# Optimization experiments

Hardware: AMD Instinct MI355X
Metric: run time of the kernel (lower is better)

The kernel has to match this reference:

```python
import jax, jax.numpy as jnp
import numpy as np

K = 24            # neighbors
RBF_KERNELS = 16
RBF_GAMMA = 10.0
CUTOFF = 5.0
BN_EPS = 1e-5


def setup_inputs() -> dict:
    key = jax.random.key(0)
    ks = jax.random.split(key, 6)
    B, C, N = 16, 32, 2048
    x = jax.random.normal(ks[0], (B, C, N), dtype=jnp.float32)
    idx_base = (jnp.arange(B, dtype=jnp.int64) * N).reshape(B, 1, 1)
    att_w1 = jax.random.normal(ks[1], (64, 2 * C + RBF_KERNELS), dtype=jnp.float32) * 0.1
    att_w2 = jax.random.normal(ks[2], (1, 64), dtype=jnp.float32) * 0.1
    upd_w = jax.random.normal(ks[3], (64, C), dtype=jnp.float32) * 0.1
    bn_gamma = jnp.ones((64,), dtype=jnp.float32)
    bn_beta = jnp.zeros((64,), dtype=jnp.float32)
    res_w = jax.random.normal(ks[4], (64, C), dtype=jnp.float32) * 0.1
    return {"x": x, "idx_base": idx_base, "att_w1": att_w1, "att_w2": att_w2,
            "upd_w": upd_w, "bn_gamma": bn_gamma, "bn_beta": bn_beta, "res_w": res_w}


def _forward(x, att_w1, att_w2, upd_w, bn_gamma, bn_beta, res_w):
    B, C, N = x.shape
    centers = jnp.linspace(0.0, CUTOFF, RBF_KERNELS).astype(x.dtype)
    # pair[b,i,j] = -||x_i - x_j||^2  (negative squared distance)
    xx = jnp.sum(x * x, axis=1)                          # [B,N]
    dots = jnp.einsum('bcn,bcm->bnm', x, x)              # [B,N,N]
    pair = 2.0 * dots - xx[:, :, None] - xx[:, None, :]
    neg_d2, idx = jax.lax.top_k(pair, K)                 # [B,N,K] nearest neighbors
    dist = jnp.sqrt(jnp.maximum(-neg_d2, 1e-12))         # [B,N,K]
    xt = jnp.transpose(x, (0, 2, 1))                     # [B,N,C]
    neigh = xt[jnp.arange(B)[:, None, None], idx]        # [B,N,K,C] gather
    cent = jnp.broadcast_to(xt[:, :, None, :], (B, N, K, C))
    # RBF expansion of neighbor distances
    diff = dist[..., None] - centers                     # [B,N,K,RBF]
    rbf = jnp.clip(jnp.exp(-RBF_GAMMA * diff * diff), 1e-10, 1.0)
    # attention MLP (1x1 convs == per-edge dense layers)
    att_in = jnp.concatenate([cent, neigh, rbf], axis=-1)          # [B,N,K,2C+RBF]
    h = jax.nn.leaky_relu(jnp.einsum('bnkf,of->bnko', att_in, att_w1), 0.2)
    logits = jnp.einsum('bnko,o->bnk', h, att_w2[0])               # [B,N,K]
    att = jax.nn.softmax(logits, axis=-1)                          # softmax over K neighbors
    weighted = att[..., None] * neigh                              # [B,N,K,C]
    # update_ff: conv1x1 -> BatchNorm2d (batch stats over B,N,K) -> LeakyReLU(0.02)
    upd = jnp.einsum('bnkc,oc->bnko', weighted, upd_w)             # [B,N,K,64]
    mean = jnp.mean(upd, axis=(0, 1, 2))
    var = jnp.mean((upd - mean) ** 2, axis=(0, 1, 2))
    upd = (upd - mean) * jax.lax.rsqrt(var + BN_EPS) * bn_gamma + bn_beta
    upd = jax.nn.leaky_relu(upd, 0.02)
    res = jnp.einsum('bnkc,oc->bnko', neigh, res_w)                # residual projection
    feat = jnp.mean(upd + 0.1 * res, axis=2)                       # mean over K -> [B,N,64]
    return jnp.transpose(feat, (0, 2, 1))                          # [B,64,N]


def reference(x, idx_base, att_w1, att_w2, upd_w, bn_gamma, bn_beta, res_w):
    # idx_base is only needed for torch's flattened-gather trick; the per-batch
    # advanced-index gather above computes identical math.
    return _forward(x, att_w1, att_w2, upd_w, bn_gamma, bn_beta, res_w)
```

## Files before the change

kernel.cpp:

```cpp
#include <hip/hip_runtime.h>
#include <math.h>

#define B_   16
#define C_   32
#define N_   2048
#define K_   24
#define BNK_ (B_*N_*K_)

typedef float vf2 __attribute__((ext_vector_type(2)));
typedef __attribute__((ext_vector_type(8))) short bf16x8;
typedef __attribute__((ext_vector_type(4))) float f32x4;

#define WS_XT   0u
#define WS_XXD  1048576u
#define WS_XXF  1114112u
#define WS_IDX  1146880u
#define WS_D2   1933312u
#define WS_ATT  2719744u
#define WS_LOG  3506176u
#define WS_ST   4292608u
#define WS_AB   4292736u
#define WS_W    4292864u
#define WS_W2   4325632u
#define WS_Y    4358400u
#define WS_L    4358400u
#define WS_HL   10649856u

__device__ __forceinline__ unsigned short bf16rne(float f) {
  unsigned int u = __float_as_uint(f);
  return (unsigned short)((u + 0x7FFFu + ((u >> 16) & 1u)) >> 16);
}

#define DPP_ADD(p, ctrl, rm)                                                  \
  (p) += __int_as_float(__builtin_amdgcn_update_dpp(                          \
      0, __float_as_int(p), (ctrl), (rm), 0xf, true))

__global__ __launch_bounds__(256) void k0_prep(const float* __restrict__ x,
                                               float* __restrict__ ws) {
  const int i = blockIdx.x;
  const int xcd = i & 7, j = i >> 3;
  const int b = 2 * xcd + (j & 1);
  const int half = j >> 1;
  const int t = (b << 11) + (half << 8) + threadIdx.x;
  const int n = t & 2047;
  const float* xp = x + ((size_t)b * C_ * N_) + n;
  float4* xt4 = (float4*)(ws + WS_XT + (size_t)t * C_);
  uint4*  hl  = (uint4*)(ws + WS_HL) + (size_t)t * 8;
  unsigned int hu[16], lu[16];
  double s = 0.0;
#pragma unroll
  for (int cg = 0; cg < 8; ++cg) {
    float4 v;
    v.x = xp[(size_t)(4*cg  ) * N_];
    v.y = xp[(size_t)(4*cg+1) * N_];
    v.z = xp[(size_t)(4*cg+2) * N_];
    v.w = xp[(size_t)(4*cg+3) * N_];
    xt4[cg] = v;
    s = fma((double)v.x, (double)v.x, s);
    s = fma((double)v.y, (double)v.y, s);
    s = fma((double)v.z, (double)v.z, s);
    s = fma((double)v.w, (double)v.w, s);
    unsigned short h0 = bf16rne(v.x), h1 = bf16rne(v.y);
    unsigned short h2 = bf16rne(v.z), h3 = bf16rne(v.w);
    float l0 = v.x - __uint_as_float((unsigned int)h0 << 16);
    float l1 = v.y - __uint_as_float((unsigned int)h1 << 16);
    float l2 = v.z - __uint_as_float((unsigned int)h2 << 16);
    float l3 = v.w - __uint_as_float((unsigned int)h3 << 16);
    hu[2*cg]   = (unsigned int)h0 | ((unsigned int)h1 << 16);
    hu[2*cg+1] = (unsigned int)h2 | ((unsigned int)h3 << 16);
    lu[2*cg]   = (unsigned int)bf16rne(l0) | ((unsigned int)bf16rne(l1) << 16);
    lu[2*cg+1] = (unsigned int)bf16rne(l2) | ((unsigned int)bf16rne(l3) << 16);
  }
#pragma unroll
  for (int q = 0; q < 4; ++q) {
    uint4 hv; hv.x = hu[4*q]; hv.y = hu[4*q+1]; hv.z = hu[4*q+2]; hv.w = hu[4*q+3];
    hl[q] = hv;
    uint4 lv; lv.x = lu[4*q]; lv.y = lu[4*q+1]; lv.z = lu[4*q+2]; lv.w = lu[4*q+3];
    hl[4+q] = lv;
  }
  ((double*)(ws + WS_XXD))[t] = s;
  ws[WS_XXF + t] = -0.5f * (float)s;
  ws[WS_W + t] = 0.f;
  ws[WS_W2 + t] = 0.f;
  if (t < 128) ws[WS_ST + t] = 0.f;
}

__global__ __launch_bounds__(256, 8) void k1a_mfma(float* __restrict__ ws) {
  __shared__ unsigned short tl[2][4096];
  const int lane = threadIdx.x & 63;
  const int wv   = __builtin_amdgcn_readfirstlane(threadIdx.x >> 6);
  const int i = blockIdx.x;
  const int xcd = i & 7, j = i >> 3;
  const int b = 2 * xcd + (j & 1);
  const int j2 = j >> 1;
  const int nblk = j2 >> 2;
  const int mq   = j2 & 3;
  const int l16 = lane & 15, lg = lane >> 4;

  const unsigned short* HL = (const unsigned short*)(ws + WS_HL) + ((size_t)b << 17);
  const int nrow = (nblk << 6) + (wv << 4) + l16;
  const bf16x8 bh = *(const bf16x8*)(HL + ((size_t)nrow << 6) + (lg << 3));
  const bf16x8 bl = *(const bf16x8*)(HL + ((size_t)nrow << 6) + 32 + (lg << 3));

  const int mbase = mq << 9;
  const float4* nxx = (const float4*)(ws + WS_XXF + (b << 11) + mbase);

  const int srow = lane >> 3;
  const int sslot = (lane & 7) ^ srow;
  const unsigned short* Sp = HL + ((size_t)(mbase + srow) << 6) + (sslot << 3);

  const int ah_off = (l16 << 6) + (((lg    ) ^ (l16 & 7)) << 3);
  const int al_off = (l16 << 6) + (((4 | lg) ^ (l16 & 7)) << 3);

  if (wv == 0) {
#pragma unroll
    for (int u = 0; u < 8; ++u) {
      const unsigned short* sp = Sp + ((size_t)(u >> 1) << 10) + (u & 1) * 512;
      __builtin_amdgcn_global_load_lds(
          (const __attribute__((address_space(1))) unsigned int*)(const void*)sp,
          (__attribute__((address_space(3))) unsigned int*)(void*)&tl[0][u * 512],
          16, 0, 0);
    }
  }
  __syncthreads();

  float val[12];
#pragma unroll
  for (int j0 = 0; j0 < 12; ++j0) val[j0] = -3.4e38f;
  int id = mbase + (lg << 2);

#pragma unroll 1
  for (int tt = 0; tt < 8; ++tt) {
    const int cur = tt & 1;
    if (tt < 7 && wv == (tt & 3)) {
#pragma unroll
      for (int u = 0; u < 8; ++u) {
        const int tile = 4 * tt + 4 + (u >> 1);
        const unsigned short* sp = Sp + ((size_t)tile << 10) + (u & 1) * 512;
        __builtin_amdgcn_global_load_lds(
            (const __attribute__((address_space(1))) unsigned int*)(const void*)sp,
            (__attribute__((address_space(3))) unsigned int*)(void*)&tl[cur ^ 1][u * 512],
            16, 0, 0);
      }
    }
#pragma unroll
    for (int sub = 0; sub < 4; ++sub) {
      const int t = 4 * tt + sub;
      const int base = sub << 10;
      bf16x8 ah = *(const bf16x8*)(&tl[cur][base + ah_off]);
      bf16x8 al = *(const bf16x8*)(&tl[cur][base + al_off]);
      float4 xq = nxx[(t << 2) + lg];
      f32x4 acc;
      acc[0] = xq.x; acc[1] = xq.y; acc[2] = xq.z; acc[3] = xq.w;
      acc = __builtin_amdgcn_mfma_f32_16x16x32_bf16(ah, bh, acc, 0, 0, 0);
      acc = __builtin_amdgcn_mfma_f32_16x16x32_bf16(al, bh, acc, 0, 0, 0);
      acc = __builtin_amdgcn_mfma_f32_16x16x32_bf16(ah, bl, acc, 0, 0, 0);
#pragma unroll
      for (int r = 0; r < 4; ++r) {
        int sb = (__float_as_int(acc[r]) & ~2047) | (id + r);
        float sp2 = __int_as_float(sb);
#pragma unroll
        for (int j0 = 11; j0 >= 1; --j0)
          val[j0] = __builtin_amdgcn_fmed3f(val[j0 - 1], val[j0], sp2);
        val[0] = fmaxf(val[0], sp2);
      }
      id += 16;
    }
    __syncthreads();
  }
  const int pg = (b << 5) + nblk;
  float* Lp = ws + WS_L +
      (((size_t)pg * 16 + (mq << 2) + lg) * 12) * 64 + (wv << 4) + l16;
#pragma unroll
  for (int j0 = 0; j0 < 12; ++j0) Lp[(size_t)j0 * 64] = val[j0];
}

__global__ __launch_bounds__(256) void k1b_sel(float* __restrict__ ws) {
  __shared__ float ls[3][28][64];
  const float* xt = ws + WS_XT;
  const double* xxd = (const double*)(ws + WS_XXD);
  const int lane = threadIdx.x & 63;
  const int wv   = threadIdx.x >> 6;
  const int i = blockIdx.x;
  const int xcd = i & 7, j = i >> 3;
  const int b = 2 * xcd + (j & 1);
  const int sub = j >> 1;
  const int pg = (b << 5) + sub;
  const int bn = (b << 11) + (sub << 6) + lane;

  float val[28];
#pragma unroll
  for (int j0 = 0; j0 < 28; ++j0) val[j0] = -3.4e38f;
  const float* Lp = ws + WS_L + ((size_t)pg * 192 + (size_t)wv * 48) * 64 + lane;
#pragma unroll 4
  for (int t = 0; t < 48; ++t) {
    float sp = Lp[(size_t)t * 64];
#pragma unroll
    for (int j0 = 27; j0 >= 1; --j0)
      val[j0] = __builtin_amdgcn_fmed3f(val[j0 - 1], val[j0], sp);
    val[0] = fmaxf(val[0], sp);
  }
  if (wv != 0) {
#pragma unroll
    for (int j0 = 0; j0 < 28; ++j0) ls[wv - 1][j0][lane] = val[j0];
  }
  __syncthreads();
  if (wv != 0) return;

#pragma unroll 1
  for (int w = 0; w < 3; ++w) {
#pragma unroll 4
    for (int t = 0; t < 28; ++t) {
      float sp = ls[w][t][lane];
#pragma unroll
      for (int j0 = 27; j0 >= 1; --j0)
        val[j0] = __builtin_amdgcn_fmed3f(val[j0 - 1], val[j0], sp);
      val[0] = fmaxf(val[0], sp);
    }
  }

  double xnd[C_];
  {
    const float* p = xt + (size_t)bn * C_;
#pragma unroll
    for (int c = 0; c < C_; ++c) xnd[c] = (double)p[c];
  }
  double dl[K_];
#pragma unroll
  for (int j0 = 0; j0 < K_; ++j0) dl[j0] = -1.7e308;

#pragma unroll 1
  for (int j0 = 0; j0 < 28; ++j0) {
    const int m = __float_as_int(val[j0]) & 2047;
    const float* r = xt + ((size_t)((b << 11) + m)) * C_;
    double a0 = 0.0, a1 = 0.0;
#pragma unroll
    for (int c = 0; c < 16; ++c) {
      a0 = fma((double)r[c],      xnd[c],      a0);
      a1 = fma((double)r[c + 16], xnd[c + 16], a1);
    }
    double s = 2.0 * (a0 + a1) - xxd[(b << 11) + m];
    long long bits = (__double_as_longlong(s) & 0xFFFFFFFFFFFFF800ll) | (long long)m;
    double sp = __longlong_as_double(bits);
    if (sp > dl[K_ - 1]) {
      bool c2 = true;
#pragma unroll
      for (int jj = K_ - 1; jj >= 1; --jj) {
        bool c1 = sp > dl[jj - 1];
        dl[jj] = c1 ? dl[jj - 1] : (c2 ? sp : dl[jj]);
        c2 = c1;
      }
      if (c2) dl[0] = sp;
    }
  }

  int*   op = (int*)ws + WS_IDX + (size_t)bn * K_;
  float* dp = ws + WS_D2 + (size_t)bn * K_;
  const double xxn = xxd[bn];
#pragma unroll
  for (int rr = 0; rr < K_; ++rr) {
    long long bl = __double_as_longlong(dl[rr]);
    op[rr] = (int)(bl & 0x7FFll);
    dp[rr] = (float)(xxn - __longlong_as_double(bl & 0xFFFFFFFFFFFFF800ll));
  }
}

__global__ __launch_bounds__(256) void kY(const float* __restrict__ w1,
                                          const float* __restrict__ updw,
                                          const float* __restrict__ resw,
                                          float* __restrict__ ws) {
  const int lane = threadIdx.x & 63;
  const int wv   = __builtin_amdgcn_readfirstlane(threadIdx.x >> 6);
  const int i = blockIdx.x;
  const int xcd = i & 7, j = i >> 3;
  const int b = 2 * xcd + (j & 1);
  const int j2 = j >> 1;
  const int slot = (j2 << 2) | wv;
  const int s  = slot & 7;
  const int pg = slot >> 3;
  const int p = (b << 11) + (pg << 6) + lane;
  const float* xt = ws + WS_XT;

  float row[C_];
  {
    const float4* rp = (const float4*)(xt + (size_t)p * C_);
#pragma unroll
    for (int q = 0; q < 8; ++q) {
      float4 v = rp[q];
      row[4*q] = v.x; row[4*q+1] = v.y; row[4*q+2] = v.z; row[4*q+3] = v.w;
    }
  }
  const int part = s >> 1;
  const int hch  = (s & 1) * 32;
  const float* W   = (part == 0) ? w1 : (part == 1) ? (w1 + 32)
                   : (part == 2) ? updw : resw;
  const int stride = (part < 2) ? 80 : 32;
  float* yp = ws + WS_Y + (size_t)p * 256 + s * 32;
#pragma unroll 2
  for (int og = 0; og < 8; ++og) {
    float a[4] = {0.f, 0.f, 0.f, 0.f};
#pragma unroll
    for (int u = 0; u < 4; ++u) {
      const float* wr = W + (hch + 4 * og + u) * stride;
#pragma unroll
      for (int c = 0; c < C_; ++c) a[u] = fmaf(row[c], wr[c], a[u]);
    }
    float4 st; st.x = a[0]; st.y = a[1]; st.z = a[2]; st.w = a[3];
    ((float4*)yp)[og] = st;
  }
}

__global__ __launch_bounds__(256, 4) void k2_logits(const float* __restrict__ w1,
                                                    const float* __restrict__ w2,
                                                    float* __restrict__ ws) {
  __shared__ unsigned short A_s[4][2048];
  __shared__ float dist_s[4][24];
  const int lane = threadIdx.x & 63;
  const int wv   = __builtin_amdgcn_readfirstlane(threadIdx.x >> 6);
  const int l16 = lane & 15, lg = lane >> 4;
  const int i = blockIdx.x;
  const int xcd = i & 7, j = i >> 3;
  const int b = 2 * xcd + (j & 1);
  const int grp = j >> 1;
  const float* Y = ws + WS_Y;

  {
    uint4 z; z.x = 0; z.y = 0; z.z = 0; z.w = 0;
    uint4* az = (uint4*)&A_s[wv][0];
    az[lane] = z; az[lane + 64] = z; az[lane + 128] = z; az[lane + 192] = z;
  }

  bf16x8 w1h[4], w1l[4];
  float w2r[4];
#pragma unroll
  for (int t = 0; t < 4; ++t) {
    const int o = t * 16 + l16;
    w2r[t] = w2[o];
    bf16x8 vh, vl;
#pragma unroll
    for (int jj = 0; jj < 8; ++jj) {
      const int r = lg * 8 + jj;
      float v = (r < 16) ? w1[o * 80 + 64 + r] : 0.f;
      unsigned short h = bf16rne(v);
      float lo = v - __uint_as_float((unsigned int)h << 16);
      vh[jj] = (short)h;
      vl[jj] = (short)bf16rne(lo);
    }
    w1h[t] = vh; w1l[t] = vl;
  }

#pragma unroll 1
  for (int q = 0; q < 4; ++q) {
    const int bn = (b << 11) + (grp << 4) + (wv << 2) + q;
    const float* dpp = ws + WS_D2 + (size_t)bn * K_;
    if (lane < K_) dist_s[wv][lane] = sqrtf(fmaxf(dpp[lane], 1e-12f));
#pragma unroll
    for (int t = 0; t < 3; ++t) {
      const int f2 = lane + (t << 6);
      const int k = f2 >> 3, r2 = f2 & 7;
      const float d = dist_s[wv][k];
      float d0 = d - (float)(2 * r2    ) * (5.0f / 15.0f);
      float d1 = d - (float)(2 * r2 + 1) * (5.0f / 15.0f);
      float e0 = fminf(fmaxf(__expf(-10.f * d0 * d0), 1e-10f), 1.0f);
      float e1 = fminf(fmaxf(__expf(-10.f * d1 * d1), 1e-10f), 1.0f);
      unsigned short h0 = bf16rne(e0), h1 = bf16rne(e1);
      float lo0 = e0 - __uint_as_float((unsigned int)h0 << 16);
      float lo1 = e1 - __uint_as_float((unsigned int)h1 << 16);
      unsigned short g0 = bf16rne(lo0), g1 = bf16rne(lo1);
      const int slot = r2 >> 2;
      const int us = (2 * r2) & 7;
      const int ph = (slot     ^ (k & 7));
      const int pl = ((4|slot) ^ (k & 7));
      *(unsigned int*)&A_s[wv][(k << 6) + (ph << 3) + us] =
          (unsigned int)h0 | ((unsigned int)h1 << 16);
      *(unsigned int*)&A_s[wv][(k << 6) + (pl << 3) + us] =
          (unsigned int)g0 | ((unsigned int)g1 << 16);
    }
    float ba[4];
#pragma unroll
    for (int t = 0; t < 4; ++t) ba[t] = Y[(size_t)bn * 256 + t * 16 + l16];

#pragma unroll
    for (int kt = 0; kt < 2; ++kt) {
      const int row = kt * 16 + l16;
      bf16x8 ah = *(const bf16x8*)&A_s[wv][(row << 6) + (((lg    ) ^ (row & 7)) << 3)];
      bf16x8 al = *(const bf16x8*)&A_s[wv][(row << 6) + (((4 | lg) ^ (row & 7)) << 3)];
      int mk[4];
#pragma unroll
      for (int reg = 0; reg < 4; ++reg) {
        const int k = kt * 16 + (lg << 2) + reg;
        mk[reg] = ((const int*)ws)[WS_IDX + (size_t)bn * K_ + (k < K_ ? k : 0)];
      }
      float sum[4] = {0.f, 0.f, 0.f, 0.f};
#pragma unroll
      for (int t = 0; t < 4; ++t) {
        f32x4 acc;
#pragma unroll
        for (int reg = 0; reg < 4; ++reg) {
          float rv = Y[(size_t)((b << 11) + mk[reg]) * 256 + 64 + t * 16 + l16];
          acc[reg] = ba[t] + rv;
        }
        acc = __builtin_amdgcn_mfma_f32_16x16x32_bf16(ah, w1h[t], acc, 0, 0, 0);
        acc = __builtin_amdgcn_mfma_f32_16x16x32_bf16(al, w1h[t], acc, 0, 0, 0);
        acc = __builtin_amdgcn_mfma_f32_16x16x32_bf16(ah, w1l[t], acc, 0, 0, 0);
#pragma unroll
        for (int reg = 0; reg < 4; ++reg) {
          float a = acc[reg];
          a = fmaxf(a, 0.2f * a);
          sum[reg] = fmaf(a, w2r[t], sum[reg]);
        }
      }
#pragma unroll
      for (int reg = 0; reg < 4; ++reg) {
        float p = sum[reg];
        DPP_ADD(p, 0xB1,  0xf);
        DPP_ADD(p, 0x4E,  0xf);
        DPP_ADD(p, 0x141, 0xf);
        DPP_ADD(p, 0x140, 0xf);
        const int k = kt * 16 + (lg << 2) + reg;
        if (l16 == 0 && k < K_) ws[WS_LOG + (size_t)k * 32768 + bn] = p;
      }
    }
  }
}

__global__ __launch_bounds__(256) void k2_softmax(float* __restrict__ ws) {
  __shared__ float h[4096];
  const int i = blockIdx.x;
  const int xcd = i & 7, j = i >> 3;
  const int b = 2 * xcd + (j & 1);
  const int half = j >> 1;
  const int bn = (b << 11) + (half << 8) + threadIdx.x;

#pragma unroll
  for (int q = 0; q < 16; ++q) h[threadIdx.x + (q << 8)] = 0.f;
  __syncthreads();

  float l[K_];
#pragma unroll
  for (int k = 0; k < K_; ++k) l[k] = ws[WS_LOG + (size_t)k * 32768 + bn];
  float mx = l[0];
#pragma unroll
  for (int k = 1; k < K_; ++k) mx = fmaxf(mx, l[k]);
  float den = 0.f;
#pragma unroll
  for (int k = 0; k < K_; ++k) { l[k] = __expf(l[k] - mx); den += l[k]; }
  const float inv = 1.f / den;
#pragma unroll
  for (int k = 0; k < K_; ++k) l[k] *= inv;

  float4* ap = (float4*)(ws + WS_ATT + (size_t)bn * K_);
#pragma unroll
  for (int q = 0; q < 6; ++q) {
    float4 v; v.x = l[4*q]; v.y = l[4*q+1]; v.z = l[4*q+2]; v.w = l[4*q+3];
    ap[q] = v;
  }
  const int* ip = (const int*)ws + WS_IDX + (size_t)bn * K_;
#pragma unroll
  for (int k = 0; k < K_; ++k) {
    const int mk = ip[k];
    atomicAdd(&h[mk], l[k]);
    atomicAdd(&h[2048 + mk], l[k] * l[k]);
  }
  __syncthreads();
#pragma unroll
  for (int q = 0; q < 8; ++q) {
    const int m = threadIdx.x + (q << 8);
    atomicAdd(ws + WS_W  + (b << 11) + m, h[m]);
    atomicAdd(ws + WS_W2 + (b << 11) + m, h[2048 + m]);
  }
}

__global__ __launch_bounds__(256) void k2b_stats(float* __restrict__ ws) {
  __shared__ float ls[128];
  const int lane = threadIdx.x & 63;
  const int wv   = __builtin_amdgcn_readfirstlane(threadIdx.x >> 6);
  if (threadIdx.x < 128) ls[threadIdx.x] = 0.f;
  __syncthreads();
  const int i = blockIdx.x;
  const int xcd = i & 7, j = i >> 3;
  const int b = 2 * xcd + (j & 1);
  const int half = j >> 1;
  const float* Y = ws + WS_Y;
  float s1 = 0.f, s2 = 0.f;
#pragma unroll 1
  for (int it = 0; it < 64; ++it) {
    const int m = (b << 11) + (half << 8) + (wv << 6) + it;
    const float w  = ws[WS_W + m];
    const float w2 = ws[WS_W2 + m];
    const float yv = Y[(size_t)m * 256 + 128 + lane];
    s1 = fmaf(w, yv, s1);
    s2 = fmaf(w2, yv * yv, s2);
  }
  atomicAdd(&ls[lane], s1);
  atomicAdd(&ls[64 + lane], s2);
  __syncthreads();
  if (threadIdx.x < 128) atomicAdd(ws + WS_ST + threadIdx.x, ls[threadIdx.x]);
}

__global__ __launch_bounds__(256) void k4_out(float* __restrict__ out,
                                              const float* __restrict__ gam,
                                              const float* __restrict__ bet,
                                              const float* __restrict__ ws) {
  __shared__ float tile[32][65];
  const int lane = threadIdx.x & 63;
  const int wv   = __builtin_amdgcn_readfirstlane(threadIdx.x >> 6);
  const int i = blockIdx.x;
  const int xcd = i & 7, j = i >> 3;
  const int b = 2 * xcd + (j & 1);
  const int j2 = j >> 1;
  const int n0 = j2 << 5;
  const float* Y = ws + WS_Y;

  float A, Bb;
  {
    const float s1 = ws[WS_ST + lane], s2 = ws[WS_ST + 64 + lane];
    const float cnt = (float)BNK_;
    const float mean = s1 / cnt;
    const float var = fmaxf(s2 / cnt - mean * mean, 0.f);
    A = gam[lane] / sqrtf(var + 1e-5f);
    Bb = bet[lane] - mean * A;
  }

#pragma unroll 1
  for (int pt = 0; pt < 8; ++pt) {
    const int bn = (b << 11) + n0 + (wv << 3) + pt;
    const int*   ip = (const int*)ws + WS_IDX + (size_t)bn * K_;
    const float* ap = ws + WS_ATT + (size_t)bn * K_;
    float facc = 0.f, racc = 0.f;
#pragma unroll
    for (int k = 0; k < K_; ++k) {
      const int mk = ip[k];
      const float* row = Y + (size_t)((b << 11) + mk) * 256;
      float yv = row[128 + lane];
      float rv = row[192 + lane];
      float u = ap[k] * yv;
      float v = fmaf(u, A, Bb);
      v = v > 0.f ? v : 0.02f * v;
      facc += v;
      racc += rv;
    }
    tile[(wv << 3) + pt][lane] = (facc + 0.1f * racc) * (1.f / 24.f);
  }
  __syncthreads();
  const int o = threadIdx.x >> 2, q = threadIdx.x & 3;
  float* op = out + ((size_t)(b * 64 + o)) * 2048 + n0 + q * 8;
  float4 v0, v1;
  v0.x = tile[q*8+0][o]; v0.y = tile[q*8+1][o]; v0.z = tile[q*8+2][o]; v0.w = tile[q*8+3][o];
  v1.x = tile[q*8+4][o]; v1.y = tile[q*8+5][o]; v1.z = tile[q*8+6][o]; v1.w = tile[q*8+7][o];
  ((float4*)op)[0] = v0;
  ((float4*)op)[1] = v1;
}

extern "C" void kernel_launch(void* const* d_in, const int* in_sizes, int n_in,
                              void* d_out, int out_size, void* d_ws, size_t ws_size,
                              hipStream_t stream) {
  (void)in_sizes; (void)n_in; (void)out_size; (void)ws_size;
  const float* x    = (const float*)d_in[0];
  const float* w1   = (const float*)d_in[2];
  const float* w2   = (const float*)d_in[3];
  const float* updw = (const float*)d_in[4];
  const float* bng  = (const float*)d_in[5];
  const float* bnb  = (const float*)d_in[6];
  const float* resw = (const float*)d_in[7];
  float* out = (float*)d_out;
  float* ws  = (float*)d_ws;

  k0_prep  <<<dim3(128),  dim3(256), 0, stream>>>(x, ws);
  k1a_mfma <<<dim3(2048), dim3(256), 0, stream>>>(ws);
  k1b_sel  <<<dim3(512),  dim3(256), 0, stream>>>(ws);
  kY       <<<dim3(1024), dim3(256), 0, stream>>>(w1, updw, resw, ws);
  k2_logits<<<dim3(2048), dim3(256), 0, stream>>>(w1, w2, ws);
  k2_softmax<<<dim3(128), dim3(256), 0, stream>>>(ws);
  k2b_stats<<<dim3(128),  dim3(256), 0, stream>>>(ws);
  k4_out   <<<dim3(1024), dim3(256), 0, stream>>>(out, bng, bnb, ws);
}
```

Measured before the change: 293.9 us.

## Parallelize candidate merge and fp64 rescoring across all four waves in k1b_sel

The cross-wave top-28 merge becomes a two-level tree reduction: waves 0 and 2 each merge a partner, then wave 0 merges wave 2's result. The fp64 rescoring of the 28 candidates is split across the four waves, seven each, and the scores go through shared memory. Only the final top-24 insertion stays on wave 0. This shortens the serial tail that used to run on a single wave, at the cost of extra shared memory and two more barriers.

```diff
diff --git a/kernel.cpp b/kernel.cpp
--- a/kernel.cpp
+++ b/kernel.cpp
@@ -176,7 +176,9 @@
 }
 
 __global__ __launch_bounds__(256) void k1b_sel(float* __restrict__ ws) {
-  __shared__ float ls[3][28][64];
+  __shared__ float  lsv[3][28][64];
+  __shared__ float  mv[28][64];
+  __shared__ double sc[28][64];
   const float* xt = ws + WS_XT;
   const double* xxd = (const double*)(ws + WS_XXD);
   const int lane = threadIdx.x & 63;
@@ -200,48 +202,70 @@
       val[j0] = __builtin_amdgcn_fmed3f(val[j0 - 1], val[j0], sp);
     val[0] = fmaxf(val[0], sp);
   }
-  if (wv != 0) {
-#pragma unroll
-    for (int j0 = 0; j0 < 28; ++j0) ls[wv - 1][j0][lane] = val[j0];
-  }
-  __syncthreads();
-  if (wv != 0) return;
-
-#pragma unroll 1
-  for (int w = 0; w < 3; ++w) {
+  if (wv == 1 || wv == 3) {
+#pragma unroll
+    for (int j0 = 0; j0 < 28; ++j0) lsv[wv >> 1][j0][lane] = val[j0];
+  }
+  __syncthreads();
+  if (wv == 0 || wv == 2) {
+    const int src = wv >> 1;
 #pragma unroll 4
     for (int t = 0; t < 28; ++t) {
-      float sp = ls[w][t][lane];
+      float sp = lsv[src][t][lane];
 #pragma unroll
       for (int j0 = 27; j0 >= 1; --j0)
         val[j0] = __builtin_amdgcn_fmed3f(val[j0 - 1], val[j0], sp);
       val[0] = fmaxf(val[0], sp);
     }
   }
-
-  double xnd[C_];
+  if (wv == 2) {
+#pragma unroll
+    for (int j0 = 0; j0 < 28; ++j0) lsv[2][j0][lane] = val[j0];
+  }
+  __syncthreads();
+  if (wv == 0) {
+#pragma unroll 4
+    for (int t = 0; t < 28; ++t) {
+      float sp = lsv[2][t][lane];
+#pragma unroll
+      for (int j0 = 27; j0 >= 1; --j0)
+        val[j0] = __builtin_amdgcn_fmed3f(val[j0 - 1], val[j0], sp);
+      val[0] = fmaxf(val[0], sp);
+    }
+#pragma unroll
+    for (int j0 = 0; j0 < 28; ++j0) mv[j0][lane] = val[j0];
+  }
+  __syncthreads();
   {
+    double xnd[C_];
     const float* p = xt + (size_t)bn * C_;
 #pragma unroll
     for (int c = 0; c < C_; ++c) xnd[c] = (double)p[c];
-  }
+#pragma unroll 1
+    for (int jj = 0; jj < 7; ++jj) {
+      const int j0 = wv * 7 + jj;
+      const int m = __float_as_int(mv[j0][lane]) & 2047;
+      const float* r = xt + ((size_t)((b << 11) + m)) * C_;
+      double a0 = 0.0, a1 = 0.0;
+#pragma unroll
+      for (int c = 0; c < 16; ++c) {
+        a0 = fma((double)r[c],      xnd[c],      a0);
+        a1 = fma((double)r[c + 16], xnd[c + 16], a1);
+      }
+      double s = 2.0 * (a0 + a1) - xxd[(b << 11) + m];
+      long long bits = (__double_as_longlong(s) & 0xFFFFFFFFFFFFF800ll) | (long long)m;
+      sc[j0][lane] = __longlong_as_double(bits);
+    }
+  }
+  __syncthreads();
+  if (wv != 0) return;
+
   double dl[K_];
 #pragma unroll
   for (int j0 = 0; j0 < K_; ++j0) dl[j0] = -1.7e308;
-
 #pragma unroll 1
   for (int j0 = 0; j0 < 28; ++j0) {
-    const int m = __float_as_int(val[j0]) & 2047;
-    const float* r = xt + ((size_t)((b << 11) + m)) * C_;
-    double a0 = 0.0, a1 = 0.0;
-#pragma unroll
-    for (int c = 0; c < 16; ++c) {
-      a0 = fma((double)r[c],      xnd[c],      a0);
-      a1 = fma((double)r[c + 16], xnd[c + 16], a1);
-    }
-    double s = 2.0 * (a0 + a1) - xxd[(b << 11) + m];
-    long long bits = (__double_as_longlong(s) & 0xFFFFFFFFFFFFF800ll) | (long long)m;
-    double sp = __longlong_as_double(bits);
+    double sp = sc[j0][lane];
     if (sp > dl[K_ - 1]) {
       bool c2 = true;
 #pragma unroll
```

After: 295.1 us. No clear change (+0.4%).
